# Kernel optimization log

Measured on AMD Instinct MI355X. Metric: run time of the kernel, lower is better.

Reference implementation:

```python
import jax, jax.numpy as jnp
import numpy as np

N_NODES = 100000
N_EDGES = 1600000


def _tconv(x, src, dst, Wq, bq, Wk, bk, Wv, bv, Ws, bs):
    """PyG TransformerConv (heads=1, concat=True, root_weight=True), eval mode."""
    n = x.shape[0]
    q = x @ Wq + bq          # [N, d]
    k = x @ Wk + bk
    v = x @ Wv + bv
    scale = 1.0 / jnp.sqrt(jnp.asarray(q.shape[1], q.dtype))
    # per-edge attention logits: query at destination, key at source
    alpha = jnp.sum(q[dst] * k[src], axis=-1) * scale       # [E]
    # segment softmax over incoming edges of each destination node
    m = jax.ops.segment_max(alpha, dst, num_segments=n)      # [N]
    e = jnp.exp(alpha - m[dst])
    s = jax.ops.segment_sum(e, dst, num_segments=n)          # [N]
    a = e / s[dst]                                           # [E]
    agg = jax.ops.segment_sum(a[:, None] * v[src], dst, num_segments=n)  # [N, d]
    return agg + x @ Ws + bs  # skip connection (root_weight=True)


def setup_inputs() -> dict:
    key = jax.random.key(0)
    ks = jax.random.split(key, 20)
    x = jax.random.normal(ks[0], (N_NODES, 2), dtype=jnp.float32)
    edge_index = jax.random.randint(ks[1], (2, N_EDGES), 0, N_NODES, dtype=jnp.int64)
    def lin(k, din, dout):
        k1, k2 = jax.random.split(k)
        lim = 1.0 / np.sqrt(din)
        W = jax.random.uniform(k1, (din, dout), jnp.float32, -lim, lim)
        b = jax.random.uniform(k2, (dout,), jnp.float32, -lim, lim)
        return W, b
    Wq1, bq1 = lin(ks[2], 2, 256)
    Wk1, bk1 = lin(ks[3], 2, 256)
    Wv1, bv1 = lin(ks[4], 2, 256)
    Ws1, bs1 = lin(ks[5], 2, 256)
    Wq2, bq2 = lin(ks[6], 256, 2)
    Wk2, bk2 = lin(ks[7], 256, 2)
    Wv2, bv2 = lin(ks[8], 256, 2)
    Ws2, bs2 = lin(ks[9], 256, 2)
    return dict(x=x, edge_index=edge_index,
                Wq1=Wq1, bq1=bq1, Wk1=Wk1, bk1=bk1, Wv1=Wv1, bv1=bv1, Ws1=Ws1, bs1=bs1,
                Wq2=Wq2, bq2=bq2, Wk2=Wk2, bk2=bk2, Wv2=Wv2, bv2=bv2, Ws2=Ws2, bs2=bs2)


def reference(x, edge_index,
              Wq1, bq1, Wk1, bk1, Wv1, bv1, Ws1, bs1,
              Wq2, bq2, Wk2, bk2, Wv2, bv2, Ws2, bs2):
    src, dst = edge_index[0], edge_index[1]
    h = _tconv(x, src, dst, Wq1, bq1, Wk1, bk1, Wv1, bv1, Ws1, bs1)
    h = jax.nn.relu(h)
    # F.dropout is identity in eval mode
    h = _tconv(h, src, dst, Wq2, bq2, Wk2, bk2, Wv2, bv2, Ws2, bs2)
    return jax.nn.log_softmax(h, axis=1)
```

## Files before the change

kernel.cpp:

```cpp
#include <hip/hip_runtime.h>


#define R_LOG2   8
#define R_DSTS   256
#define BE       4096
#define MAXNB    512
#define CAPB     4608
#define S_SLICES 4
#define RSQRT2   0.70710678118654752f

__global__ void coeff_k(const float* __restrict__ Wq1, const float* __restrict__ bq1,
                        const float* __restrict__ Wk1, const float* __restrict__ bk1,
                        float* __restrict__ coeff) {
    __shared__ float part[4][9];
    int c = threadIdx.x;
    float wq0 = Wq1[c], wq1 = Wq1[256 + c];
    float wk0 = Wk1[c], wk1 = Wk1[256 + c];
    float bq = bq1[c], bk = bk1[c];
    float vals[9] = { wq0 * wk0, wq0 * wk1, wq1 * wk0, wq1 * wk1,
                      wq0 * bk,  wq1 * bk,  bq * wk0,  bq * wk1,  bq * bk };
    int lane = c & 63, w = c >> 6;
#pragma unroll
    for (int i = 0; i < 9; ++i) {
        float v = vals[i];
#pragma unroll
        for (int o = 32; o > 0; o >>= 1) v += __shfl_xor(v, o);
        if (lane == 0) part[w][i] = v;
    }
    __syncthreads();
    if (c < 9) coeff[c] = part[0][c] + part[1][c] + part[2][c] + part[3][c];
}

__global__ __launch_bounds__(256) void scatter1_k(
        const int* __restrict__ src, const int* __restrict__ dst,
        int* __restrict__ cnt, int* __restrict__ recs, int NB, int E) {
    __shared__ int hist[MAXNB];
    __shared__ int lofs[MAXNB];
    __shared__ int gbase[MAXNB];
    __shared__ int stage[BE];
    __shared__ unsigned short sbkt[BE];
    __shared__ int wsum[4];
    int t = threadIdx.x;
    for (int i = t; i < NB; i += 256) hist[i] = 0;
    __syncthreads();

    int base = blockIdx.x * BE;
    int nloc = E - base; if (nloc > BE) nloc = BE;
    int nv = nloc >> 2;
    const int4* d4 = (const int4*)(dst + base);
    const int4* s4 = (const int4*)(src + base);

    for (int i = t; i < nv; i += 256) {
        int4 v = d4[i];
        atomicAdd(&hist[v.x >> R_LOG2], 1);
        atomicAdd(&hist[v.y >> R_LOG2], 1);
        atomicAdd(&hist[v.z >> R_LOG2], 1);
        atomicAdd(&hist[v.w >> R_LOG2], 1);
    }
    for (int i = (nv << 2) + t; i < nloc; i += 256)
        atomicAdd(&hist[dst[base + i] >> R_LOG2], 1);
    __syncthreads();

    {
        int i0 = 2 * t, i1 = 2 * t + 1;
        int a = (i0 < NB) ? hist[i0] : 0;
        int b = (i1 < NB) ? hist[i1] : 0;
        int s = a + b;
        int lane = t & 63, w = t >> 6;
        int incl = s;
#pragma unroll
        for (int o = 1; o < 64; o <<= 1) {
            int u = __shfl_up(incl, o);
            if (lane >= o) incl += u;
        }
        if (lane == 63) wsum[w] = incl;
        __syncthreads();
        int ex = incl - s;
        for (int j = 0; j < w; ++j) ex += wsum[j];
        if (i0 < NB) lofs[i0] = ex;
        if (i1 < NB) lofs[i1] = ex + a;
    }
    __syncthreads();

    for (int b = t; b < NB; b += 256) {
        int h = hist[b];
        int start = h ? atomicAdd(&cnt[b], h) : 0;
        gbase[b] = b * CAPB + start - lofs[b];
        hist[b] = 0;
    }
    __syncthreads();

    for (int i = t; i < nv; i += 256) {
        int4 dv = d4[i];
        int4 sv = s4[i];
        int d, b, r, p;
        d = dv.x; b = d >> R_LOG2; r = atomicAdd(&hist[b], 1); p = lofs[b] + r;
        stage[p] = sv.x | ((d & (R_DSTS - 1)) << 17); sbkt[p] = (unsigned short)b;
        d = dv.y; b = d >> R_LOG2; r = atomicAdd(&hist[b], 1); p = lofs[b] + r;
        stage[p] = sv.y | ((d & (R_DSTS - 1)) << 17); sbkt[p] = (unsigned short)b;
        d = dv.z; b = d >> R_LOG2; r = atomicAdd(&hist[b], 1); p = lofs[b] + r;
        stage[p] = sv.z | ((d & (R_DSTS - 1)) << 17); sbkt[p] = (unsigned short)b;
        d = dv.w; b = d >> R_LOG2; r = atomicAdd(&hist[b], 1); p = lofs[b] + r;
        stage[p] = sv.w | ((d & (R_DSTS - 1)) << 17); sbkt[p] = (unsigned short)b;
    }
    for (int i = (nv << 2) + t; i < nloc; i += 256) {
        int d = dst[base + i];
        int b = d >> R_LOG2;
        int r = atomicAdd(&hist[b], 1);
        int p = lofs[b] + r;
        stage[p] = src[base + i] | ((d & (R_DSTS - 1)) << 17);
        sbkt[p] = (unsigned short)b;
    }
    __syncthreads();

    for (int i = t; i < nloc; i += 256) {
        int bk = sbkt[i];
        int p = gbase[bk] + i;
        if (p < (bk + 1) * CAPB) recs[p] = stage[i];
    }
}

__global__ __launch_bounds__(256) void l1r_k(
        const float* __restrict__ x, const float* __restrict__ coeff,
        const int* __restrict__ recs, const int* __restrict__ cnt,
        float* __restrict__ part, int N) {
    __shared__ float p0[R_DSTS], p1[R_DSTS], pc[R_DSTS];
    __shared__ float ac[3 * R_DSTS];
    int t = threadIdx.x;
    int bs = blockIdx.x;
    int b = bs >> 2;
    int sl = bs & 3;
    int nbase = b << R_LOG2;
    int rem = N - nbase; if (rem > R_DSTS) rem = R_DSTS;

    ac[t] = 0.f; ac[256 + t] = 0.f; ac[512 + t] = 0.f;
    if (t < rem) {
        float2 xd = ((const float2*)x)[nbase + t];
        float c0 = coeff[0], c1 = coeff[1], c2 = coeff[2], c3 = coeff[3];
        float c4 = coeff[4], c5 = coeff[5], c6 = coeff[6], c7 = coeff[7];
        float c8 = coeff[8];
        p0[t] = c0 * xd.x + c2 * xd.y + c6;
        p1[t] = c1 * xd.x + c3 * xd.y + c7;
        pc[t] = c4 * xd.x + c5 * xd.y + c8;
    }
    __syncthreads();

    int cb = cnt[b]; if (cb > CAPB) cb = CAPB;
    int len = (cb + S_SLICES - 1) / S_SLICES;
    int lo = sl * len;
    int hi = lo + len; if (hi > cb) hi = cb;
    const int* rb = recs + (size_t)b * CAPB;
    for (int i = lo + t; i < hi; i += 256) {
        int rec = rb[i];
        int s = rec & 0x1FFFF;
        int dl = (rec >> 17) & (R_DSTS - 1);
        float2 xs = ((const float2*)x)[s];
        float w = __expf((p0[dl] * xs.x + p1[dl] * xs.y + pc[dl]) * 0.0625f);
        atomicAdd(&ac[dl], w);
        atomicAdd(&ac[256 + dl], w * xs.x);
        atomicAdd(&ac[512 + dl], w * xs.y);
    }
    __syncthreads();

    float* dp = part + (size_t)bs * (3 * R_DSTS);
    dp[t] = ac[t];
    dp[256 + t] = ac[256 + t];
    dp[512 + t] = ac[512 + t];
}

__global__ __launch_bounds__(256, 3) void proj_k(
        const float* __restrict__ x, const float* __restrict__ part,
        const float* __restrict__ Wv1, const float* __restrict__ bv1,
        const float* __restrict__ Ws1, const float* __restrict__ bs1,
        const float* __restrict__ Wq2, const float* __restrict__ bq2,
        const float* __restrict__ Wk2, const float* __restrict__ bk2,
        const float* __restrict__ Wv2, const float* __restrict__ bv2,
        const float* __restrict__ Ws2, const float* __restrict__ bs2,
        float* __restrict__ q2, float4* __restrict__ kv2,
        float* __restrict__ hs2, int N) {
    __shared__ float sW[14][256];
    int t = threadIdx.x;
    sW[0][t]  = Wv1[t];
    sW[1][t]  = Wv1[256 + t];
    sW[2][t]  = Ws1[t];
    sW[3][t]  = Ws1[256 + t];
    sW[4][t]  = bv1[t];
    sW[5][t]  = bs1[t];
    sW[6][t]  = Wq2[2 * t];
    sW[7][t]  = Wq2[2 * t + 1];
    sW[8][t]  = Wk2[2 * t];
    sW[9][t]  = Wk2[2 * t + 1];
    sW[10][t] = Wv2[2 * t];
    sW[11][t] = Wv2[2 * t + 1];
    sW[12][t] = Ws2[2 * t];
    sW[13][t] = Ws2[2 * t + 1];
    __syncthreads();

    int g = t & 7;
    int grp = t >> 3;
    int nb = blockIdx.x * 128 + grp * 4;

    float a0[4], a1[4], he[4], xdx[4], xdy[4];
#pragma unroll
    for (int k = 0; k < 4; ++k) {
        int n = nb + k;
        float s = 0.f, sx0 = 0.f, sx1 = 0.f;
        if (n < N) {
            int b = n >> R_LOG2, idx = n & (R_DSTS - 1);
            const float* pp = part + ((size_t)(b * S_SLICES + (g & 3))) * (3 * R_DSTS) + idx;
            s = pp[0]; sx0 = pp[256]; sx1 = pp[512];
        }
#pragma unroll
        for (int m = 1; m < 4; m <<= 1) {
            s   += __shfl_xor(s, m);
            sx0 += __shfl_xor(sx0, m);
            sx1 += __shfl_xor(sx1, m);
        }
        a0[k] = 0.f; a1[k] = 0.f; he[k] = 0.f;
        if (s > 0.f) {
            float inv = 1.0f / s;
            a0[k] = sx0 * inv; a1[k] = sx1 * inv; he[k] = 1.f;
        }
        float2 xd = make_float2(0.f, 0.f);
        if (n < N) xd = ((const float2*)x)[n];
        xdx[k] = xd.x; xdy[k] = xd.y;
    }

    float acc[4][8];
#pragma unroll
    for (int k = 0; k < 4; ++k)
#pragma unroll
        for (int i = 0; i < 8; ++i) acc[k][i] = 0.f;

#pragma unroll 1
    for (int j = 0; j < 8; ++j) {
        int ci = g + 8 * j;
        float4 hk[4];
        {
            float4 w0 = ((const float4*)sW[0])[ci];
            float4 w1 = ((const float4*)sW[1])[ci];
            float4 w2 = ((const float4*)sW[2])[ci];
            float4 w3 = ((const float4*)sW[3])[ci];
            float4 w4 = ((const float4*)sW[4])[ci];
            float4 w5 = ((const float4*)sW[5])[ci];
#pragma unroll
            for (int k = 0; k < 4; ++k) {
                hk[k].x = fmaxf(a0[k]*w0.x + a1[k]*w1.x + xdx[k]*w2.x + xdy[k]*w3.x + he[k]*w4.x + w5.x, 0.f);
                hk[k].y = fmaxf(a0[k]*w0.y + a1[k]*w1.y + xdx[k]*w2.y + xdy[k]*w3.y + he[k]*w4.y + w5.y, 0.f);
                hk[k].z = fmaxf(a0[k]*w0.z + a1[k]*w1.z + xdx[k]*w2.z + xdy[k]*w3.z + he[k]*w4.z + w5.z, 0.f);
                hk[k].w = fmaxf(a0[k]*w0.w + a1[k]*w1.w + xdx[k]*w2.w + xdy[k]*w3.w + he[k]*w4.w + w5.w, 0.f);
            }
        }
#pragma unroll
        for (int i = 0; i < 8; ++i) {
            float4 u = ((const float4*)sW[6 + i])[ci];
#pragma unroll
            for (int k = 0; k < 4; ++k)
                acc[k][i] += hk[k].x*u.x + hk[k].y*u.y + hk[k].z*u.z + hk[k].w*u.w;
        }
    }
#pragma unroll
    for (int k = 0; k < 4; ++k)
#pragma unroll
        for (int i = 0; i < 8; ++i) {
#pragma unroll
            for (int m = 1; m < 8; m <<= 1)
                acc[k][i] += __shfl_xor(acc[k][i], m);
        }
    if (g < 4) {
        int n = nb + g;
        if (n < N) {
            ((float2*)q2)[n]  = make_float2(acc[g][0] + bq2[0], acc[g][1] + bq2[1]);
            kv2[n] = make_float4(acc[g][2] + bk2[0], acc[g][3] + bk2[1],
                                 acc[g][4] + bv2[0], acc[g][5] + bv2[1]);
            ((float2*)hs2)[n] = make_float2(acc[g][6] + bs2[0], acc[g][7] + bs2[1]);
        }
    }
}

__global__ __launch_bounds__(256) void l2r_k(
        const float* __restrict__ q2, const float4* __restrict__ kv2,
        const int* __restrict__ recs, const int* __restrict__ cnt,
        float* __restrict__ part, int N) {
    __shared__ float qx[R_DSTS], qy[R_DSTS];
    __shared__ float ac[3 * R_DSTS];
    int t = threadIdx.x;
    int bs = blockIdx.x;
    int b = bs >> 2;
    int sl = bs & 3;
    int nbase = b << R_LOG2;
    int rem = N - nbase; if (rem > R_DSTS) rem = R_DSTS;

    ac[t] = 0.f; ac[256 + t] = 0.f; ac[512 + t] = 0.f;
    if (t < rem) {
        float2 q = ((const float2*)q2)[nbase + t];
        qx[t] = q.x * RSQRT2;
        qy[t] = q.y * RSQRT2;
    }
    __syncthreads();

    int cb = cnt[b]; if (cb > CAPB) cb = CAPB;
    int len = (cb + S_SLICES - 1) / S_SLICES;
    int lo = sl * len;
    int hi = lo + len; if (hi > cb) hi = cb;
    const int* rb = recs + (size_t)b * CAPB;
    for (int i = lo + t; i < hi; i += 256) {
        int rec = rb[i];
        int s = rec & 0x1FFFF;
        int dl = (rec >> 17) & (R_DSTS - 1);
        float4 kv = kv2[s];
        float w = __expf(qx[dl] * kv.x + qy[dl] * kv.y);
        atomicAdd(&ac[dl], w);
        atomicAdd(&ac[256 + dl], w * kv.z);
        atomicAdd(&ac[512 + dl], w * kv.w);
    }
    __syncthreads();

    float* dp = part + (size_t)bs * (3 * R_DSTS);
    dp[t] = ac[t];
    dp[256 + t] = ac[256 + t];
    dp[512 + t] = ac[512 + t];
}

__global__ __launch_bounds__(256) void out2x_k(
        const float* __restrict__ part, const float* __restrict__ hs2,
        float* __restrict__ out, int N) {
    int t = threadIdx.x;
    int g = t & 7;
    int n = blockIdx.x * 32 + (t >> 3);
    if (n >= N) return;
    int b = n >> R_LOG2, idx = n & (R_DSTS - 1);

    const float* pp = part + ((size_t)(b * S_SLICES + (g & 3))) * (3 * R_DSTS) + idx;
    float s = pp[0], sv0 = pp[256], sv1 = pp[512];
#pragma unroll
    for (int m = 1; m < 4; m <<= 1) {
        s   += __shfl_xor(s, m);
        sv0 += __shfl_xor(sv0, m);
        sv1 += __shfl_xor(sv1, m);
    }
    if (g != 0) return;

    float g0 = 0.f, g1 = 0.f;
    if (s > 0.f) {
        float inv = 1.0f / s;
        g0 = sv0 * inv; g1 = sv1 * inv;
    }
    float2 hs = ((const float2*)hs2)[n];
    float o0 = g0 + hs.x;
    float o1 = g1 + hs.y;
    float mx = fmaxf(o0, o1), mn = fminf(o0, o1);
    float lse = mx + log1pf(__expf(mn - mx));
    ((float2*)out)[n] = make_float2(o0 - lse, o1 - lse);
}

extern "C" void kernel_launch(void* const* d_in, const int* in_sizes, int n_in,
                              void* d_out, int out_size, void* d_ws, size_t ws_size,
                              hipStream_t stream) {
    const float* x   = (const float*)d_in[0];
    const int*   ei  = (const int*)d_in[1];
    const float* Wq1 = (const float*)d_in[2];
    const float* bq1 = (const float*)d_in[3];
    const float* Wk1 = (const float*)d_in[4];
    const float* bk1 = (const float*)d_in[5];
    const float* Wv1 = (const float*)d_in[6];
    const float* bv1 = (const float*)d_in[7];
    const float* Ws1 = (const float*)d_in[8];
    const float* bs1 = (const float*)d_in[9];
    const float* Wq2 = (const float*)d_in[10];
    const float* bq2 = (const float*)d_in[11];
    const float* Wk2 = (const float*)d_in[12];
    const float* bk2 = (const float*)d_in[13];
    const float* Wv2 = (const float*)d_in[14];
    const float* bv2 = (const float*)d_in[15];
    const float* Ws2 = (const float*)d_in[16];
    const float* bs2 = (const float*)d_in[17];

    const int N = in_sizes[0] / 2;
    const int E = in_sizes[1] / 2;
    const int* src = ei;
    const int* dst = ei + E;

    const int NB   = (N + R_DSTS - 1) >> R_LOG2;
    const int NBlk = (E + BE - 1) / BE;

    float* ws = (float*)d_ws;
    size_t off = 0;
    float* coeff = ws + off;                 off += 16;
    int*   cnt   = (int*)(ws + off);         off += NB;
    int*   recs  = (int*)(ws + off);         off += (size_t)NB * CAPB;
    off = (off + 3) & ~(size_t)3;
    float* part  = ws + off;                 off += (size_t)NB * S_SLICES * 3 * R_DSTS;
    float4* kv2  = (float4*)(ws + off);      off += 4 * (size_t)N;
    float* q2    = ws + off;                 off += 2 * (size_t)N;
    float* hs2   = ws + off;                 off += 2 * (size_t)N;

    const int gP  = (N + 127) / 128;
    const int gO  = (N + 31) / 32;

    hipMemsetAsync(cnt, 0, NB * sizeof(int), stream);
    coeff_k<<<1, 256, 0, stream>>>(Wq1, bq1, Wk1, bk1, coeff);
    scatter1_k<<<NBlk, 256, 0, stream>>>(src, dst, cnt, recs, NB, E);
    l1r_k<<<NB * S_SLICES, 256, 0, stream>>>(x, coeff, recs, cnt, part, N);
    proj_k<<<gP, 256, 0, stream>>>(x, part, Wv1, bv1, Ws1, bs1,
                                   Wq2, bq2, Wk2, bk2, Wv2, bv2, Ws2, bs2,
                                   q2, kv2, hs2, N);
    l2r_k<<<NB * S_SLICES, 256, 0, stream>>>(q2, kv2, recs, cnt, part, N);
    out2x_k<<<gO, 256, 0, stream>>>(part, hs2, (float*)d_out, N);
}
```

Measured before the change: 127.8 us.

## Fold coeff kernel into l1r, widen scatter blocks, shrink proj per-thread work

Removes the single-block coeff kernel: every l1r block now recomputes the nine Wq1·Wk1 coefficients itself, which saves one launch and a dependency. scatter1 goes from 256 to 1024 threads per block with one histogram bin per thread, giving more parallelism in the scan and bucketing phases. proj_k handles 2 nodes per 8-thread group instead of 4 and its launch bound asks for 4 blocks instead of 3, trading weight reuse for occupancy and more blocks. The cost is redundant coefficient work in each l1r block and more shared-memory atomic contention with the larger scatter blocks.

Result: faster. 123.0 us (-3.8%).

```diff
diff --git a/kernel.cpp b/kernel.cpp
--- a/kernel.cpp
+++ b/kernel.cpp
@@ -9,29 +9,7 @@
 #define S_SLICES 4
 #define RSQRT2   0.70710678118654752f
 
-__global__ void coeff_k(const float* __restrict__ Wq1, const float* __restrict__ bq1,
-                        const float* __restrict__ Wk1, const float* __restrict__ bk1,
-                        float* __restrict__ coeff) {
-    __shared__ float part[4][9];
-    int c = threadIdx.x;
-    float wq0 = Wq1[c], wq1 = Wq1[256 + c];
-    float wk0 = Wk1[c], wk1 = Wk1[256 + c];
-    float bq = bq1[c], bk = bk1[c];
-    float vals[9] = { wq0 * wk0, wq0 * wk1, wq1 * wk0, wq1 * wk1,
-                      wq0 * bk,  wq1 * bk,  bq * wk0,  bq * wk1,  bq * bk };
-    int lane = c & 63, w = c >> 6;
-#pragma unroll
-    for (int i = 0; i < 9; ++i) {
-        float v = vals[i];
-#pragma unroll
-        for (int o = 32; o > 0; o >>= 1) v += __shfl_xor(v, o);
-        if (lane == 0) part[w][i] = v;
-    }
-    __syncthreads();
-    if (c < 9) coeff[c] = part[0][c] + part[1][c] + part[2][c] + part[3][c];
-}
-
-__global__ __launch_bounds__(256) void scatter1_k(
+__global__ __launch_bounds__(1024) void scatter1_k(
         const int* __restrict__ src, const int* __restrict__ dst,
         int* __restrict__ cnt, int* __restrict__ recs, int NB, int E) {
     __shared__ int hist[MAXNB];
@@ -39,9 +17,9 @@
     __shared__ int gbase[MAXNB];
     __shared__ int stage[BE];
     __shared__ unsigned short sbkt[BE];
-    __shared__ int wsum[4];
+    __shared__ int wsum[16];
     int t = threadIdx.x;
-    for (int i = t; i < NB; i += 256) hist[i] = 0;
+    if (t < NB) hist[t] = 0;
     __syncthreads();
 
     int base = blockIdx.x * BE;
@@ -50,24 +28,21 @@
     const int4* d4 = (const int4*)(dst + base);
     const int4* s4 = (const int4*)(src + base);
 
-    for (int i = t; i < nv; i += 256) {
+    for (int i = t; i < nv; i += 1024) {
         int4 v = d4[i];
         atomicAdd(&hist[v.x >> R_LOG2], 1);
         atomicAdd(&hist[v.y >> R_LOG2], 1);
         atomicAdd(&hist[v.z >> R_LOG2], 1);
         atomicAdd(&hist[v.w >> R_LOG2], 1);
     }
-    for (int i = (nv << 2) + t; i < nloc; i += 256)
+    for (int i = (nv << 2) + t; i < nloc; i += 1024)
         atomicAdd(&hist[dst[base + i] >> R_LOG2], 1);
     __syncthreads();
 
     {
-        int i0 = 2 * t, i1 = 2 * t + 1;
-        int a = (i0 < NB) ? hist[i0] : 0;
-        int b = (i1 < NB) ? hist[i1] : 0;
-        int s = a + b;
+        int v = (t < NB) ? hist[t] : 0;
         int lane = t & 63, w = t >> 6;
-        int incl = s;
+        int incl = v;
 #pragma unroll
         for (int o = 1; o < 64; o <<= 1) {
             int u = __shfl_up(incl, o);
@@ -75,22 +50,21 @@
         }
         if (lane == 63) wsum[w] = incl;
         __syncthreads();
-        int ex = incl - s;
+        int ex = incl - v;
         for (int j = 0; j < w; ++j) ex += wsum[j];
-        if (i0 < NB) lofs[i0] = ex;
-        if (i1 < NB) lofs[i1] = ex + a;
-    }
-    __syncthreads();
-
-    for (int b = t; b < NB; b += 256) {
-        int h = hist[b];
-        int start = h ? atomicAdd(&cnt[b], h) : 0;
-        gbase[b] = b * CAPB + start - lofs[b];
-        hist[b] = 0;
-    }
-    __syncthreads();
-
-    for (int i = t; i < nv; i += 256) {
+        if (t < NB) lofs[t] = ex;
+    }
+    __syncthreads();
+
+    if (t < NB) {
+        int h = hist[t];
+        int start = h ? atomicAdd(&cnt[t], h) : 0;
+        gbase[t] = t * CAPB + start - lofs[t];
+        hist[t] = 0;
+    }
+    __syncthreads();
+
+    for (int i = t; i < nv; i += 1024) {
         int4 dv = d4[i];
         int4 sv = s4[i];
         int d, b, r, p;
@@ -103,7 +77,7 @@
         d = dv.w; b = d >> R_LOG2; r = atomicAdd(&hist[b], 1); p = lofs[b] + r;
         stage[p] = sv.w | ((d & (R_DSTS - 1)) << 17); sbkt[p] = (unsigned short)b;
     }
-    for (int i = (nv << 2) + t; i < nloc; i += 256) {
+    for (int i = (nv << 2) + t; i < nloc; i += 1024) {
         int d = dst[base + i];
         int b = d >> R_LOG2;
         int r = atomicAdd(&hist[b], 1);
@@ -113,7 +87,7 @@
     }
     __syncthreads();
 
-    for (int i = t; i < nloc; i += 256) {
+    for (int i = t; i < nloc; i += 1024) {
         int bk = sbkt[i];
         int p = gbase[bk] + i;
         if (p < (bk + 1) * CAPB) recs[p] = stage[i];
@@ -121,12 +95,36 @@
 }
 
 __global__ __launch_bounds__(256) void l1r_k(
-        const float* __restrict__ x, const float* __restrict__ coeff,
+        const float* __restrict__ x,
+        const float* __restrict__ Wq1, const float* __restrict__ bq1,
+        const float* __restrict__ Wk1, const float* __restrict__ bk1,
         const int* __restrict__ recs, const int* __restrict__ cnt,
         float* __restrict__ part, int N) {
     __shared__ float p0[R_DSTS], p1[R_DSTS], pc[R_DSTS];
     __shared__ float ac[3 * R_DSTS];
+    __shared__ float cpart[4][9];
+    __shared__ float c9[9];
     int t = threadIdx.x;
+
+    {
+        float wq0 = Wq1[t], wq1 = Wq1[256 + t];
+        float wk0 = Wk1[t], wk1 = Wk1[256 + t];
+        float bq = bq1[t], bk = bk1[t];
+        float vals[9] = { wq0 * wk0, wq0 * wk1, wq1 * wk0, wq1 * wk1,
+                          wq0 * bk,  wq1 * bk,  bq * wk0,  bq * wk1,  bq * bk };
+        int lane = t & 63, w = t >> 6;
+#pragma unroll
+        for (int i = 0; i < 9; ++i) {
+            float v = vals[i];
+#pragma unroll
+            for (int o = 32; o > 0; o >>= 1) v += __shfl_xor(v, o);
+            if (lane == 0) cpart[w][i] = v;
+        }
+        __syncthreads();
+        if (t < 9) c9[t] = cpart[0][t] + cpart[1][t] + cpart[2][t] + cpart[3][t];
+        __syncthreads();
+    }
+
     int bs = blockIdx.x;
     int b = bs >> 2;
     int sl = bs & 3;
@@ -136,12 +134,9 @@
     ac[t] = 0.f; ac[256 + t] = 0.f; ac[512 + t] = 0.f;
     if (t < rem) {
         float2 xd = ((const float2*)x)[nbase + t];
-        float c0 = coeff[0], c1 = coeff[1], c2 = coeff[2], c3 = coeff[3];
-        float c4 = coeff[4], c5 = coeff[5], c6 = coeff[6], c7 = coeff[7];
-        float c8 = coeff[8];
-        p0[t] = c0 * xd.x + c2 * xd.y + c6;
-        p1[t] = c1 * xd.x + c3 * xd.y + c7;
-        pc[t] = c4 * xd.x + c5 * xd.y + c8;
+        p0[t] = c9[0] * xd.x + c9[2] * xd.y + c9[6];
+        p1[t] = c9[1] * xd.x + c9[3] * xd.y + c9[7];
+        pc[t] = c9[4] * xd.x + c9[5] * xd.y + c9[8];
     }
     __syncthreads();
 
@@ -168,7 +163,7 @@
     dp[512 + t] = ac[512 + t];
 }
 
-__global__ __launch_bounds__(256, 3) void proj_k(
+__global__ __launch_bounds__(256, 4) void proj_k(
         const float* __restrict__ x, const float* __restrict__ part,
         const float* __restrict__ Wv1, const float* __restrict__ bv1,
         const float* __restrict__ Ws1, const float* __restrict__ bs1,
@@ -198,11 +193,11 @@
 
     int g = t & 7;
     int grp = t >> 3;
-    int nb = blockIdx.x * 128 + grp * 4;
-
-    float a0[4], a1[4], he[4], xdx[4], xdy[4];
-#pragma unroll
-    for (int k = 0; k < 4; ++k) {
+    int nb = blockIdx.x * 64 + grp * 2;
+
+    float a0[2], a1[2], he[2], xdx[2], xdy[2];
+#pragma unroll
+    for (int k = 0; k < 2; ++k) {
         int n = nb + k;
         float s = 0.f, sx0 = 0.f, sx1 = 0.f;
         if (n < N) {
@@ -226,16 +221,16 @@
         xdx[k] = xd.x; xdy[k] = xd.y;
     }
 
-    float acc[4][8];
-#pragma unroll
-    for (int k = 0; k < 4; ++k)
+    float acc[2][8];
+#pragma unroll
+    for (int k = 0; k < 2; ++k)
 #pragma unroll
         for (int i = 0; i < 8; ++i) acc[k][i] = 0.f;
 
 #pragma unroll 1
     for (int j = 0; j < 8; ++j) {
         int ci = g + 8 * j;
-        float4 hk[4];
+        float4 hk[2];
         {
             float4 w0 = ((const float4*)sW[0])[ci];
             float4 w1 = ((const float4*)sW[1])[ci];
@@ -244,7 +239,7 @@
             float4 w4 = ((const float4*)sW[4])[ci];
             float4 w5 = ((const float4*)sW[5])[ci];
 #pragma unroll
-            for (int k = 0; k < 4; ++k) {
+            for (int k = 0; k < 2; ++k) {
                 hk[k].x = fmaxf(a0[k]*w0.x + a1[k]*w1.x + xdx[k]*w2.x + xdy[k]*w3.x + he[k]*w4.x + w5.x, 0.f);
                 hk[k].y = fmaxf(a0[k]*w0.y + a1[k]*w1.y + xdx[k]*w2.y + xdy[k]*w3.y + he[k]*w4.y + w5.y, 0.f);
                 hk[k].z = fmaxf(a0[k]*w0.z + a1[k]*w1.z + xdx[k]*w2.z + xdy[k]*w3.z + he[k]*w4.z + w5.z, 0.f);
@@ -255,19 +250,19 @@
         for (int i = 0; i < 8; ++i) {
             float4 u = ((const float4*)sW[6 + i])[ci];
 #pragma unroll
-            for (int k = 0; k < 4; ++k)
+            for (int k = 0; k < 2; ++k)
                 acc[k][i] += hk[k].x*u.x + hk[k].y*u.y + hk[k].z*u.z + hk[k].w*u.w;
         }
     }
 #pragma unroll
-    for (int k = 0; k < 4; ++k)
+    for (int k = 0; k < 2; ++k)
 #pragma unroll
         for (int i = 0; i < 8; ++i) {
 #pragma unroll
             for (int m = 1; m < 8; m <<= 1)
                 acc[k][i] += __shfl_xor(acc[k][i], m);
         }
-    if (g < 4) {
+    if (g < 2) {
         int n = nb + g;
         if (n < N) {
             ((float2*)q2)[n]  = make_float2(acc[g][0] + bq2[0], acc[g][1] + bq2[1]);
@@ -386,7 +381,6 @@
 
     float* ws = (float*)d_ws;
     size_t off = 0;
-    float* coeff = ws + off;                 off += 16;
     int*   cnt   = (int*)(ws + off);         off += NB;
     int*   recs  = (int*)(ws + off);         off += (size_t)NB * CAPB;
     off = (off + 3) & ~(size_t)3;
@@ -395,13 +389,13 @@
     float* q2    = ws + off;                 off += 2 * (size_t)N;
     float* hs2   = ws + off;                 off += 2 * (size_t)N;
 
-    const int gP  = (N + 127) / 128;
+    const int gP  = (N + 63) / 64;
     const int gO  = (N + 31) / 32;
 
     hipMemsetAsync(cnt, 0, NB * sizeof(int), stream);
-    coeff_k<<<1, 256, 0, stream>>>(Wq1, bq1, Wk1, bk1, coeff);
-    scatter1_k<<<NBlk, 256, 0, stream>>>(src, dst, cnt, recs, NB, E);
-    l1r_k<<<NB * S_SLICES, 256, 0, stream>>>(x, coeff, recs, cnt, part, N);
+    scatter1_k<<<NBlk, 1024, 0, stream>>>(src, dst, cnt, recs, NB, E);
+    l1r_k<<<NB * S_SLICES, 256, 0, stream>>>(x, Wq1, bq1, Wk1, bk1,
+                                             recs, cnt, part, N);
     proj_k<<<gP, 256, 0, stream>>>(x, part, Wv1, bv1, Ws1, bs1,
                                    Wq2, bq2, Wk2, bk2, Wv2, bv2, Ws2, bs2,
                                    q2, kv2, hs2, N);
```
